# Optimization experiments

Hardware: AMD Instinct MI355X
Metric: run time of the kernel (lower is better)

Reference implementation:

```python
import jax, jax.numpy as jnp
import numpy as np

EMBED = 1024
HEADS = 16
HDIM = EMBED // HEADS
MASK_OUT = -10000.0


def setup_inputs() -> dict:
    key = jax.random.key(0)
    ks = jax.random.split(key, 12)
    B, S = 4, 1023
    scale = 0.02
    return {
        "word_hidden_states": jax.random.normal(ks[0], (B, S, EMBED), jnp.float32),
        "image_hidden_states": jax.random.normal(ks[1], (B, EMBED), jnp.float32),
        "attention_mask": jnp.zeros((B, 1, 1, S), jnp.float32),
        "c_attn_w": jax.random.normal(ks[2], (EMBED, 3 * EMBED), jnp.float32) * scale,
        "c_attn_b": jnp.zeros((3 * EMBED,), jnp.float32),
        "c_proj_w": jax.random.normal(ks[3], (EMBED, EMBED), jnp.float32) * scale,
        "c_proj_b": jnp.zeros((EMBED,), jnp.float32),
        "uk_w": jax.random.normal(ks[4], (EMBED, EMBED), jnp.float32) * scale,
        "uk_b": jnp.zeros((EMBED,), jnp.float32),
        "uv_w": jax.random.normal(ks[5], (EMBED, EMBED), jnp.float32) * scale,
        "uv_b": jnp.zeros((EMBED,), jnp.float32),
    }


def _split_heads(t):
    # [B, T, E] -> [B, H, T, D]
    B, T, _ = t.shape
    return t.reshape(B, T, HEADS, HDIM).transpose(0, 2, 1, 3)


def reference(word_hidden_states, image_hidden_states, attention_mask,
              c_attn_w, c_attn_b, c_proj_w, c_proj_b,
              uk_w, uk_b, uv_w, uv_b):
    B, S, _ = word_hidden_states.shape
    # c_attn: Conv1D -> x @ W + b, then split into q, k, v
    qkv = word_hidden_states @ c_attn_w + c_attn_b          # [B, S, 3E]
    q_word, k_word, v_word = jnp.split(qkv, 3, axis=-1)
    # image key/value via nn.Linear (x @ W^T + b)
    img = image_hidden_states[:, None, :]                    # [B, 1, E]
    k_img = img @ uk_w.T + uk_b
    v_img = img @ uv_w.T + uv_b
    k = jnp.concatenate([k_img, k_word], axis=1)             # [B, S+1, E]
    v = jnp.concatenate([v_img, v_word], axis=1)

    q = _split_heads(q_word)                                 # [B, H, S, D]
    k = _split_heads(k)                                      # [B, H, S+1, D]
    v = _split_heads(v)

    scores = jnp.einsum("bhqd,bhkd->bhqk", q, k) / jnp.sqrt(jnp.float32(HDIM))
    # causal mask: tril rows [1 : S+1], cols [: S+1] of max_positions grid
    # -> query i may attend key j iff j <= i + 1 (image token always visible)
    qi = jnp.arange(S)[:, None]
    kj = jnp.arange(S + 1)[None, :]
    causal = kj <= qi + 1                                     # [S, S+1]
    scores = jnp.where(causal[None, None], scores, jnp.float32(MASK_OUT))
    # prepend zero column to additive attention mask for the image token
    zero_col = jnp.zeros(attention_mask.shape[:-1] + (1,), attention_mask.dtype)
    mask = jnp.concatenate([zero_col, attention_mask], axis=-1)  # [B,1,1,S+1]
    scores = scores + mask
    attn = jax.nn.softmax(scores, axis=-1)                    # dropout: eval mode (identity)
    out = jnp.einsum("bhqk,bhkd->bhqd", attn, v)              # [B, H, S, D]
    out = out.transpose(0, 2, 1, 3).reshape(B, S, EMBED)      # merge heads
    out = out @ c_proj_w + c_proj_b                           # c_proj Conv1D
    return out
```

## Files before the change

### kernel.cpp

```cpp
#include <hip/hip_runtime.h>

#define EMBED 1024
#define HEADS 16
#define HDIM 64
#define SQ 1023
#define SK 1024
#define MTOK 4092
#define MPAD 4096

typedef __attribute__((ext_vector_type(8))) short short8;
typedef __attribute__((ext_vector_type(4))) float floatx4;

static __device__ __forceinline__ unsigned short f2bf(float f) {
  union { float f; unsigned u; } v; v.f = f;
  unsigned u = v.u;
  u += 0x7fffu + ((u >> 16) & 1u);
  return (unsigned short)(u >> 16);
}
static __device__ __forceinline__ float bf2f(unsigned short s) {
  union { unsigned u; float f; } v; v.u = ((unsigned)s) << 16;
  return v.f;
}

static __device__ __forceinline__ void gld16(const unsigned short* g, unsigned short* l) {
  typedef const __attribute__((address_space(1))) unsigned int guint;
  typedef __attribute__((address_space(3))) unsigned int luint;
  __builtin_amdgcn_global_load_lds((guint*)(const void*)g, (luint*)(void*)l, 16, 0, 0);
}

__global__ __launch_bounds__(256) void k_prep(
    const float* __restrict__ word, const float* __restrict__ attn_w,
    const float* __restrict__ proj_w, const float* __restrict__ img,
    const float* __restrict__ ukw, const float* __restrict__ ukb,
    const float* __restrict__ uvw, const float* __restrict__ uvb,
    unsigned short* __restrict__ A, unsigned short* __restrict__ WtA,
    unsigned short* __restrict__ WtP, unsigned short* __restrict__ Qb,
    unsigned short* __restrict__ Kb, unsigned short* __restrict__ Vt) {
  __shared__ float T[32][33];
  int bx = blockIdx.x, t = threadIdx.x;
  if (bx < 2048) {
    int idx = (bx * 256 + t) * 8;
    int row = idx >> 10;
    short8 v;
    if (row < MTOK) {
      const float4* p = (const float4*)(word + idx);
      float4 a = p[0], b = p[1];
      v[0] = (short)f2bf(a.x); v[1] = (short)f2bf(a.y);
      v[2] = (short)f2bf(a.z); v[3] = (short)f2bf(a.w);
      v[4] = (short)f2bf(b.x); v[5] = (short)f2bf(b.y);
      v[6] = (short)f2bf(b.z); v[7] = (short)f2bf(b.w);
    } else {
#pragma unroll
      for (int i = 0; i < 8; i++) v[i] = 0;
    }
    *(short8*)(A + idx) = v;
  } else if (bx < 6144) {
    const float* W; unsigned short* Wt; int N, n0, k0;
    if (bx < 5120) {
      int r = bx - 2048; W = attn_w; Wt = WtA; N = 3072;
      n0 = (r % 96) * 32; k0 = (r / 96) * 32;
    } else {
      int r = bx - 5120; W = proj_w; Wt = WtP; N = 1024;
      n0 = (r & 31) * 32; k0 = (r >> 5) * 32;
    }
    int tx = t & 31, ty = t >> 5;
#pragma unroll
    for (int i = 0; i < 4; i++) {
      int r = ty + i * 8;
      T[r][tx] = W[(k0 + r) * N + n0 + tx];
    }
    __syncthreads();
#pragma unroll
    for (int i = 0; i < 4; i++) {
      int r = ty + i * 8;
      Wt[(n0 + r) * 1024 + k0 + tx] = f2bf(T[tx][r]);
    }
  } else if (bx < 8192) {
    int wid = (bx - 6144) * 4 + (t >> 6);
    int lane = t & 63;
    int which = wid >> 12;
    int bb = (wid >> 10) & 3;
    int n = wid & 1023;
    const float* W = which ? uvw : ukw;
    const float* bias = which ? uvb : ukb;
    const float* x = img + bb * 1024;
    const float* w = W + n * 1024;
    float s = 0.f;
#pragma unroll
    for (int i = 0; i < 16; i++) { int k = i * 64 + lane; s += x[k] * w[k]; }
#pragma unroll
    for (int off = 32; off; off >>= 1) s += __shfl_xor(s, off);
    if (lane == 0) {
      int h = n >> 6, d = n & 63;
      unsigned short val = f2bf(s + bias[n]);
      if (which == 0) Kb[((bb * HEADS + h) * SK + (SK - 1)) * HDIM + d] = val;
      else            Vt[((bb * HEADS + h) * HDIM + d) * SK + (SK - 1)] = val;
    }
  } else {
    int i = (bx - 8192) * 256 + t;
    int bh = i >> 6, d = i & 63;
    Qb[(bh * SK + (SK - 1)) * HDIM + d] = 0;
  }
}

template <int EPI>
__global__ __launch_bounds__(256, 2) void k_gemm(
    const unsigned short* __restrict__ A, const unsigned short* __restrict__ Bt,
    int Kdim, const float* __restrict__ bias,
    unsigned short* __restrict__ Qb, unsigned short* __restrict__ Kb,
    unsigned short* __restrict__ VtOut, float* __restrict__ out) {
  __shared__ __attribute__((aligned(16))) unsigned short Sm[16384];
  unsigned short* As = Sm;
  unsigned short* Bs = Sm + 8192;
  int t = threadIdx.x, lane = t & 63, w = t >> 6;
  int quad = lane >> 4, l16 = lane & 15;
  int m0 = blockIdx.y * 128, n0 = blockIdx.x * 128;
  int waveM = (w >> 1) * 64, waveN = (w & 1) * 64;
  int rs = t >> 3, cs = t & 7;

  floatx4 acc[4][4];
#pragma unroll
  for (int i = 0; i < 4; i++)
#pragma unroll
    for (int j = 0; j < 4; j++)
#pragma unroll
      for (int e = 0; e < 4; e++) acc[i][j][e] = 0.f;

  const unsigned short* Ag = A + m0 * Kdim;
  const unsigned short* Bg = Bt + n0 * Kdim;

  for (int k0 = 0; k0 < Kdim; k0 += 64) {
    __syncthreads();
#pragma unroll
    for (int i = 0; i < 4; i++) {
      int r = i * 32 + rs;
      gld16(Ag + r * Kdim + k0 + ((cs ^ (r & 7)) * 8), As + i * 2048 + t * 8);
    }
#pragma unroll
    for (int i = 0; i < 4; i++) {
      int r = i * 32 + rs;
      gld16(Bg + r * Kdim + k0 + ((cs ^ (r & 7)) * 8), Bs + i * 2048 + t * 8);
    }
    __syncthreads();
    short8 af[2][4], bf8[2][4];
#pragma unroll
    for (int kk = 0; kk < 2; kk++) {
#pragma unroll
      for (int mr = 0; mr < 4; mr++) {
        int row = waveM + mr * 16 + l16;
        af[kk][mr] = *(const short8*)(As + row * 64 + (((kk * 4 + quad) ^ (row & 7)) * 8));
      }
#pragma unroll
      for (int nc = 0; nc < 4; nc++) {
        int row = waveN + nc * 16 + l16;
        bf8[kk][nc] = *(const short8*)(Bs + row * 64 + (((kk * 4 + quad) ^ (row & 7)) * 8));
      }
    }
#pragma unroll
    for (int kk = 0; kk < 2; kk++)
#pragma unroll
      for (int mr = 0; mr < 4; mr++)
#pragma unroll
        for (int nc = 0; nc < 4; nc++)
          acc[mr][nc] = __builtin_amdgcn_mfma_f32_16x16x32_bf16(af[kk][mr], bf8[kk][nc], acc[mr][nc], 0, 0, 0);
  }

  float bv[4];
#pragma unroll
  for (int nc = 0; nc < 4; nc++) bv[nc] = bias[n0 + waveN + nc * 16 + l16];

  if (EPI == 0) {
    unsigned short* Cs = Sm;
    int which0 = n0 >> 10;
    for (int p = 0; p < 2; p++) {
      __syncthreads();
      if ((w >> 1) == p) {
#pragma unroll
        for (int mr = 0; mr < 4; mr++)
#pragma unroll
          for (int nc = 0; nc < 4; nc++)
#pragma unroll
            for (int r = 0; r < 4; r++) {
              int lrow = mr * 16 + quad * 4 + r;
              int lcol = waveN + nc * 16 + l16;
              Cs[lrow * 128 + ((((lcol >> 3) + lrow) & 15) * 8) + (lcol & 7)] =
                  f2bf(acc[mr][nc][r] + bv[nc]);
            }
      }
      __syncthreads();
      if (which0 == 2) {
        int tok = t & 63;
        int gm = m0 + p * 64 + tok;
        int cb = (t >> 6) * 32;
        bool okm = (gm < MTOK);
        int bb = (unsigned)gm / 1023u;
        int s = gm - bb * 1023;
#pragma unroll
        for (int it = 0; it < 32; it++) {
          int c = cb + it;
          unsigned short val = Cs[tok * 128 + ((((c >> 3) + tok) & 15) * 8) + (c & 7)];
          int e = (n0 + c) & 1023;
          int h = e >> 6, d0 = e & 63;
          if (okm) VtOut[((bb * HEADS + h) * HDIM + d0) * SK + s] = val;
        }
      } else {
        unsigned short* dst = which0 ? Kb : Qb;
#pragma unroll
        for (int i = 0; i < 4; i++) {
          int cid = i * 256 + t;
          int lr = cid >> 4, c8 = cid & 15;
          short8 v = *(const short8*)(Cs + lr * 128 + (((c8 + lr) & 15) * 8));
          int gm = m0 + p * 64 + lr;
          if (gm < MTOK) {
            int gn = n0 + c8 * 8;
            int e = gn & 1023;
            int h = e >> 6, d0 = e & 63;
            int bb = (unsigned)gm / 1023u;
            int s = gm - bb * 1023;
            *(short8*)(dst + ((bb * HEADS + h) * SK + s) * HDIM + d0) = v;
          }
        }
      }
    }
  } else {
#pragma unroll
    for (int nc = 0; nc < 4; nc++) {
      int gn = n0 + waveN + nc * 16 + l16;
#pragma unroll
      for (int mr = 0; mr < 4; mr++) {
#pragma unroll
        for (int r = 0; r < 4; r++) {
          int gm = m0 + waveM + mr * 16 + quad * 4 + r;
          if (gm < MTOK) out[gm * EMBED + gn] = acc[mr][nc][r] + bv[nc];
        }
      }
    }
  }
}

__global__ __launch_bounds__(256, 2) void k_flash(
    const unsigned short* __restrict__ Qb, const unsigned short* __restrict__ Kb,
    const unsigned short* __restrict__ Vtg, const float* __restrict__ am,
    unsigned short* __restrict__ Ao) {
  __shared__ __attribute__((aligned(16))) unsigned short Ks[8192];
  __shared__ __attribute__((aligned(16))) unsigned short Vs[8192];
  __shared__ __attribute__((aligned(16))) unsigned short Ps[8192];

  int t = threadIdx.x, lane = t & 63, w = t >> 6;
  int quad = lane >> 4, l16 = lane & 15;
  int B = blockIdx.x;
  int bh = (B & 7) | (((B >> 3) & 7) << 3);
  int tq = 15 - (B >> 6);
  int bb = bh >> 4, h = bh & 15;

  const float SCL = 0.18033688011f;
  const float MASKV = -14426.950408f;
  const float L2E = 1.44269504089f;

  short8 qf[2];
  {
    int qrow = tq * 64 + w * 16 + l16;
#pragma unroll
    for (int kk = 0; kk < 2; kk++)
      qf[kk] = *(const short8*)(Qb + (bh * SK + qrow) * HDIM + (kk * 4 + quad) * 8);
  }

  float m_i[4], l_i[4];
  floatx4 acc_o[4];
  {
    float s0 = 0.f;
#pragma unroll
    for (int kk = 0; kk < 2; kk++) {
      short8 ki = *(const short8*)(Kb + (bh * SK + (SK - 1)) * HDIM + (kk * 4 + quad) * 8);
#pragma unroll
      for (int j = 0; j < 8; j++)
        s0 += bf2f((unsigned short)qf[kk][j]) * bf2f((unsigned short)ki[j]);
    }
    s0 += __shfl_xor(s0, 16);
    s0 += __shfl_xor(s0, 32);
    s0 *= SCL;
#pragma unroll
    for (int r = 0; r < 4; r++) {
      m_i[r] = __shfl(s0, quad * 4 + r);
      l_i[r] = 1.f;
    }
#pragma unroll
    for (int n = 0; n < 4; n++) {
      float vf = bf2f(Vtg[(bh * HDIM + n * 16 + l16) * SK + (SK - 1)]);
#pragma unroll
      for (int e = 0; e < 4; e++) acc_o[n][e] = vf;
    }
  }

  unsigned short* Pw = Ps + w * 2048;
  const float* amb = am + bb * SQ;
  int jmax = tq >> 1;

  for (int j = 0; j <= jmax; j++) {
    __syncthreads();
#pragma unroll
    for (int i = 0; i < 4; i++) {
      int r = i * 32 + (t >> 3), gc = (t & 7) ^ (r & 7);
      gld16(Kb + (bh * SK + j * 128 + r) * HDIM + gc * 8, Ks + i * 2048 + t * 8);
    }
#pragma unroll
    for (int i = 0; i < 4; i++) {
      int d = i * 16 + (t >> 4), gc = (t & 15) ^ (d & 7);
      gld16(Vtg + (bh * HDIM + d) * SK + j * 128 + gc * 8, Vs + i * 2048 + t * 8);
    }
    __syncthreads();

    bool diag = (j == jmax);
    int qmaxw = tq * 64 + w * 16 + 15;

    floatx4 sacc[8];
#pragma unroll
    for (int n = 0; n < 8; n++)
#pragma unroll
      for (int e = 0; e < 4; e++) sacc[n][e] = 0.f;
#pragma unroll
    for (int nc = 0; nc < 8; nc++) {
      if (j * 128 + nc * 16 <= qmaxw) {
        int krow = nc * 16 + l16;
#pragma unroll
        for (int kk = 0; kk < 2; kk++) {
          short8 b = *(const short8*)(Ks + krow * 64 + (((kk * 4 + quad) ^ (krow & 7)) * 8));
          sacc[nc] = __builtin_amdgcn_mfma_f32_16x16x32_bf16(qf[kk], b, sacc[nc], 0, 0, 0);
        }
      }
    }

    int qbase = tq * 64 + w * 16 + quad * 4;
    float tmax[4];
#pragma unroll
    for (int r = 0; r < 4; r++) tmax[r] = -1e30f;
#pragma unroll
    for (int nc = 0; nc < 8; nc++) {
      if (j * 128 + nc * 16 > qmaxw) {
#pragma unroll
        for (int r = 0; r < 4; r++) sacc[nc][r] = 0.f;
      } else {
        int s = j * 128 + nc * 16 + l16;
        float amv = (s < SQ) ? amb[s] * L2E : 0.f;
#pragma unroll
        for (int r = 0; r < 4; r++) {
          float sc = sacc[nc][r] * SCL;
          if (diag && s > qbase + r) sc = MASKV;
          sc += amv;
          sacc[nc][r] = sc;
          tmax[r] = fmaxf(tmax[r], sc);
        }
      }
    }
#pragma unroll
    for (int off = 1; off < 16; off <<= 1)
#pragma unroll
      for (int r = 0; r < 4; r++) tmax[r] = fmaxf(tmax[r], __shfl_xor(tmax[r], off));

    float alpha[4];
#pragma unroll
    for (int r = 0; r < 4; r++) {
      float mn = fmaxf(m_i[r], tmax[r]);
      alpha[r] = __builtin_amdgcn_exp2f(m_i[r] - mn);
      m_i[r] = mn;
    }
    float rsum[4] = {0.f, 0.f, 0.f, 0.f};
#pragma unroll
    for (int nc = 0; nc < 8; nc++) {
      if (j * 128 + nc * 16 <= qmaxw) {
#pragma unroll
        for (int r = 0; r < 4; r++) {
          float p = __builtin_amdgcn_exp2f(sacc[nc][r] - m_i[r]);
          sacc[nc][r] = p;
          rsum[r] += p;
        }
      }
    }
#pragma unroll
    for (int off = 1; off < 16; off <<= 1)
#pragma unroll
      for (int r = 0; r < 4; r++) rsum[r] += __shfl_xor(rsum[r], off);
#pragma unroll
    for (int r = 0; r < 4; r++) l_i[r] = l_i[r] * alpha[r] + rsum[r];
#pragma unroll
    for (int n = 0; n < 4; n++)
#pragma unroll
      for (int e = 0; e < 4; e++) acc_o[n][e] *= alpha[e];

#pragma unroll
    for (int nc = 0; nc < 8; nc++)
#pragma unroll
      for (int r = 0; r < 4; r++) {
        int row = quad * 4 + r;
        union { float f; unsigned u; } cv; cv.f = sacc[nc][r];
        Pw[row * 128 + (((nc * 2 + (l16 >> 3)) ^ (row & 7)) * 8) + (l16 & 7)] =
            (unsigned short)(cv.u >> 16);
      }

#pragma unroll
    for (int kk2 = 0; kk2 < 4; kk2++) {
      short8 a = *(const short8*)(Pw + l16 * 128 + (((kk2 * 4 + quad) ^ (l16 & 7)) * 8));
#pragma unroll
      for (int n = 0; n < 4; n++) {
        int vrow = n * 16 + l16;
        short8 b = *(const short8*)(Vs + vrow * 128 + (((kk2 * 4 + quad) ^ (vrow & 7)) * 8));
        acc_o[n] = __builtin_amdgcn_mfma_f32_16x16x32_bf16(a, b, acc_o[n], 0, 0, 0);
      }
    }
  }

  float inv[4];
#pragma unroll
  for (int r = 0; r < 4; r++) inv[r] = 1.f / l_i[r];
  unsigned short* Os = Ps;
  __syncthreads();
#pragma unroll
  for (int n = 0; n < 4; n++)
#pragma unroll
    for (int r = 0; r < 4; r++) {
      int row = w * 16 + quad * 4 + r, col = n * 16 + l16;
      Os[row * 64 + ((((col >> 3) + row) & 7) * 8) + (col & 7)] = f2bf(acc_o[n][r] * inv[r]);
    }
  __syncthreads();
#pragma unroll
  for (int i = 0; i < 2; i++) {
    int cid = i * 256 + t, r = cid >> 3, c8 = cid & 7;
    int q = tq * 64 + r;
    if (q < SQ) {
      short8 v = *(const short8*)(Os + r * 64 + (((c8 + r) & 7) * 8));
      *(short8*)(Ao + (bb * SQ + q) * EMBED + h * HDIM + c8 * 8) = v;
    }
  }
}

extern "C" void kernel_launch(void* const* d_in, const int* in_sizes, int n_in,
                              void* d_out, int out_size, void* d_ws, size_t ws_size,
                              hipStream_t stream) {
  const float* word   = (const float*)d_in[0];
  const float* img    = (const float*)d_in[1];
  const float* amask  = (const float*)d_in[2];
  const float* attn_w = (const float*)d_in[3];
  const float* attn_b = (const float*)d_in[4];
  const float* proj_w = (const float*)d_in[5];
  const float* proj_b = (const float*)d_in[6];
  const float* ukw    = (const float*)d_in[7];
  const float* ukb    = (const float*)d_in[8];
  const float* uvw    = (const float*)d_in[9];
  const float* uvb    = (const float*)d_in[10];
  float* out = (float*)d_out;

  char* ws = (char*)d_ws;
  unsigned short* Aw     = (unsigned short*)(ws);
  unsigned short* WtAttn = (unsigned short*)(ws + 8388608);
  unsigned short* WtProj = (unsigned short*)(ws + 14680064);
  unsigned short* Qb     = (unsigned short*)(ws + 16777216);
  unsigned short* Kb     = (unsigned short*)(ws + 25165824);
  unsigned short* Vtg    = (unsigned short*)(ws + 33554432);
  unsigned short* Ao     = Aw;

  k_prep<<<8208, 256, 0, stream>>>(word, attn_w, proj_w, img, ukw, ukb, uvw, uvb,
                                   Aw, WtAttn, WtProj, Qb, Kb, Vtg);
  k_gemm<0><<<dim3(24, 32), 256, 0, stream>>>(Aw, WtAttn, 1024, attn_b, Qb, Kb, Vtg, nullptr);
  k_flash<<<1024, 256, 0, stream>>>(Qb, Kb, Vtg, amask, Ao);
  k_gemm<1><<<dim3(8, 32), 256, 0, stream>>>(Ao, WtProj, 1024, proj_b, nullptr, nullptr, nullptr, out);
}
```

Measured before the change: 209.2 us.

## Widen QKV GEMM N-tile to 192 and unify mixed Q/K/V epilogue

Templates the GEMM on N-tile width and launches the QKV projection with 192-wide tiles (16x32 blocks instead of 24x32), so the grid fits in fewer waves on the CUs. Because a 192-wide tile can straddle the Q/K and V regions, the epilogue is rewritten to handle vectorized Q/K stores and scalar transposed V stores within one block. It also uses a padded XOR-swizzled staging layout and loads fragments per k-step to limit registers. The cost is more registers and LDS per block and a less uniform epilogue.

```diff
diff --git a/kernel.cpp b/kernel.cpp
--- a/kernel.cpp
+++ b/kernel.cpp
@@ -103,26 +103,27 @@
   }
 }
 
-template <int EPI>
+template <int EPI, int TN>
 __global__ __launch_bounds__(256, 2) void k_gemm(
     const unsigned short* __restrict__ A, const unsigned short* __restrict__ Bt,
     int Kdim, const float* __restrict__ bias,
     unsigned short* __restrict__ Qb, unsigned short* __restrict__ Kb,
     unsigned short* __restrict__ VtOut, float* __restrict__ out) {
-  __shared__ __attribute__((aligned(16))) unsigned short Sm[16384];
+  constexpr int NC = TN / 32;
+  __shared__ __attribute__((aligned(16))) unsigned short Sm[8192 + TN * 64];
   unsigned short* As = Sm;
   unsigned short* Bs = Sm + 8192;
   int t = threadIdx.x, lane = t & 63, w = t >> 6;
   int quad = lane >> 4, l16 = lane & 15;
-  int m0 = blockIdx.y * 128, n0 = blockIdx.x * 128;
-  int waveM = (w >> 1) * 64, waveN = (w & 1) * 64;
+  int m0 = blockIdx.y * 128, n0 = blockIdx.x * TN;
+  int waveM = (w >> 1) * 64, waveN = (w & 1) * (TN / 2);
   int rs = t >> 3, cs = t & 7;
 
-  floatx4 acc[4][4];
+  floatx4 acc[4][NC];
 #pragma unroll
   for (int i = 0; i < 4; i++)
 #pragma unroll
-    for (int j = 0; j < 4; j++)
+    for (int j = 0; j < NC; j++)
 #pragma unroll
       for (int e = 0; e < 4; e++) acc[i][j][e] = 0.f;
 
@@ -137,94 +138,91 @@
       gld16(Ag + r * Kdim + k0 + ((cs ^ (r & 7)) * 8), As + i * 2048 + t * 8);
     }
 #pragma unroll
-    for (int i = 0; i < 4; i++) {
+    for (int i = 0; i < TN / 32; i++) {
       int r = i * 32 + rs;
       gld16(Bg + r * Kdim + k0 + ((cs ^ (r & 7)) * 8), Bs + i * 2048 + t * 8);
     }
     __syncthreads();
-    short8 af[2][4], bf8[2][4];
 #pragma unroll
     for (int kk = 0; kk < 2; kk++) {
+      short8 af[4], bf8[NC];
 #pragma unroll
       for (int mr = 0; mr < 4; mr++) {
         int row = waveM + mr * 16 + l16;
-        af[kk][mr] = *(const short8*)(As + row * 64 + (((kk * 4 + quad) ^ (row & 7)) * 8));
-      }
-#pragma unroll
-      for (int nc = 0; nc < 4; nc++) {
+        af[mr] = *(const short8*)(As + row * 64 + (((kk * 4 + quad) ^ (row & 7)) * 8));
+      }
+#pragma unroll
+      for (int nc = 0; nc < NC; nc++) {
         int row = waveN + nc * 16 + l16;
-        bf8[kk][nc] = *(const short8*)(Bs + row * 64 + (((kk * 4 + quad) ^ (row & 7)) * 8));
-      }
-    }
-#pragma unroll
-    for (int kk = 0; kk < 2; kk++)
+        bf8[nc] = *(const short8*)(Bs + row * 64 + (((kk * 4 + quad) ^ (row & 7)) * 8));
+      }
 #pragma unroll
       for (int mr = 0; mr < 4; mr++)
 #pragma unroll
-        for (int nc = 0; nc < 4; nc++)
-          acc[mr][nc] = __builtin_amdgcn_mfma_f32_16x16x32_bf16(af[kk][mr], bf8[kk][nc], acc[mr][nc], 0, 0, 0);
-  }
-
-  float bv[4];
-#pragma unroll
-  for (int nc = 0; nc < 4; nc++) bv[nc] = bias[n0 + waveN + nc * 16 + l16];
+        for (int nc = 0; nc < NC; nc++)
+          acc[mr][nc] = __builtin_amdgcn_mfma_f32_16x16x32_bf16(af[mr], bf8[nc], acc[mr][nc], 0, 0, 0);
+    }
+  }
+
+  float bv[NC];
+#pragma unroll
+  for (int nc = 0; nc < NC; nc++) bv[nc] = bias[n0 + waveN + nc * 16 + l16];
 
   if (EPI == 0) {
     unsigned short* Cs = Sm;
-    int which0 = n0 >> 10;
+    const int CST = 208;
+    int startV = 2048 - n0;
+    if (startV < 0) startV = 0;
+    if (startV > TN) startV = TN;
+    int chunksQK = startV >> 3;
     for (int p = 0; p < 2; p++) {
       __syncthreads();
       if ((w >> 1) == p) {
 #pragma unroll
         for (int mr = 0; mr < 4; mr++)
 #pragma unroll
-          for (int nc = 0; nc < 4; nc++)
+          for (int nc = 0; nc < NC; nc++)
 #pragma unroll
             for (int r = 0; r < 4; r++) {
               int lrow = mr * 16 + quad * 4 + r;
               int lcol = waveN + nc * 16 + l16;
-              Cs[lrow * 128 + ((((lcol >> 3) + lrow) & 15) * 8) + (lcol & 7)] =
+              Cs[lrow * CST + (((lcol >> 3) ^ (quad << 1)) * 8) + (lcol & 7)] =
                   f2bf(acc[mr][nc][r] + bv[nc]);
             }
       }
       __syncthreads();
-      if (which0 == 2) {
-        int tok = t & 63;
-        int gm = m0 + p * 64 + tok;
-        int cb = (t >> 6) * 32;
+      {
+        int lr = t & 63, gm = m0 + p * 64 + lr;
+        int rot = ((lr >> 2) & 3) << 1;
         bool okm = (gm < MTOK);
         int bb = (unsigned)gm / 1023u;
         int s = gm - bb * 1023;
-#pragma unroll
-        for (int it = 0; it < 32; it++) {
-          int c = cb + it;
-          unsigned short val = Cs[tok * 128 + ((((c >> 3) + tok) & 15) * 8) + (c & 7)];
+        for (int c8 = (t >> 6); c8 < chunksQK; c8 += 4) {
+          short8 v = *(const short8*)(Cs + lr * CST + ((c8 ^ rot) * 8));
+          int gn = n0 + c8 * 8;
+          unsigned short* dst = (gn >> 10) ? Kb : Qb;
+          int e = gn & 1023;
+          int h = e >> 6, d0 = e & 63;
+          if (okm) *(short8*)(dst + ((bb * HEADS + h) * SK + s) * HDIM + d0) = v;
+        }
+      }
+      {
+        int tok = t & 63, gm = m0 + p * 64 + tok;
+        int rot = ((tok >> 2) & 3) << 1;
+        bool okm = (gm < MTOK);
+        int bb = (unsigned)gm / 1023u;
+        int s = gm - bb * 1023;
+        for (int c = startV + (t >> 6); c < TN; c += 4) {
+          unsigned short val = Cs[tok * CST + (((c >> 3) ^ rot) * 8) + (c & 7)];
           int e = (n0 + c) & 1023;
           int h = e >> 6, d0 = e & 63;
           if (okm) VtOut[((bb * HEADS + h) * HDIM + d0) * SK + s] = val;
         }
-      } else {
-        unsigned short* dst = which0 ? Kb : Qb;
-#pragma unroll
-        for (int i = 0; i < 4; i++) {
-          int cid = i * 256 + t;
-          int lr = cid >> 4, c8 = cid & 15;
-          short8 v = *(const short8*)(Cs + lr * 128 + (((c8 + lr) & 15) * 8));
-          int gm = m0 + p * 64 + lr;
-          if (gm < MTOK) {
-            int gn = n0 + c8 * 8;
-            int e = gn & 1023;
-            int h = e >> 6, d0 = e & 63;
-            int bb = (unsigned)gm / 1023u;
-            int s = gm - bb * 1023;
-            *(short8*)(dst + ((bb * HEADS + h) * SK + s) * HDIM + d0) = v;
-          }
-        }
       }
     }
   } else {
 #pragma unroll
-    for (int nc = 0; nc < 4; nc++) {
+    for (int nc = 0; nc < NC; nc++) {
       int gn = n0 + waveN + nc * 16 + l16;
 #pragma unroll
       for (int mr = 0; mr < 4; mr++) {
@@ -460,7 +458,7 @@
 
   k_prep<<<8208, 256, 0, stream>>>(word, attn_w, proj_w, img, ukw, ukb, uvw, uvb,
                                    Aw, WtAttn, WtProj, Qb, Kb, Vtg);
-  k_gemm<0><<<dim3(24, 32), 256, 0, stream>>>(Aw, WtAttn, 1024, attn_b, Qb, Kb, Vtg, nullptr);
+  k_gemm<0, 192><<<dim3(16, 32), 256, 0, stream>>>(Aw, WtAttn, 1024, attn_b, Qb, Kb, Vtg, nullptr);
   k_flash<<<1024, 256, 0, stream>>>(Qb, Kb, Vtg, amask, Ao);
-  k_gemm<1><<<dim3(8, 32), 256, 0, stream>>>(Ao, WtProj, 1024, proj_b, nullptr, nullptr, nullptr, out);
-}
+  k_gemm<1, 128><<<dim3(8, 32), 256, 0, stream>>>(Ao, WtProj, 1024, proj_b, nullptr, nullptr, nullptr, out);
+}
```

Measured after the change: 202.8 us. 3.1% less time.
